# Kernel optimization log

Hardware: AMD Instinct MI355X
Metric: run time of the kernel (lower is better)

Reference implementation:

```python
import jax, jax.numpy as jnp
import numpy as np

N = 16384
D = 128
TOPK = 32


def setup_inputs() -> dict:
    key = jax.random.key(0)
    kx, kw = jax.random.split(key)
    x = jax.random.normal(kx, (N,), dtype=jnp.float32)  # unused by the module's forward
    W = jax.random.normal(kw, (N, D), dtype=jnp.float32)  # embedding table (learned param)
    return {"x": x, "W": W}


def reference(x, W):
    # adj = E @ E^T : [N, N] similarity matrix
    adj = W @ W.T
    # per-row top-K (torch.topk along dim=1)
    vals, idx = jax.lax.top_k(adj, TOPK)  # [N, K] each
    # dense_to_sparse emits nonzeros in row-major order -> sort columns within each row.
    order = jnp.argsort(idx, axis=1)
    idx_s = jnp.take_along_axis(idx, order, axis=1)
    vals_s = jnp.take_along_axis(vals, order, axis=1)
    rows = jnp.repeat(jnp.arange(N, dtype=idx_s.dtype), TOPK)
    edge_index = jnp.stack([rows, idx_s.reshape(-1)])  # [2, N*K]
    edge_values = vals_s.reshape(-1)  # [N*K]
    return edge_index, edge_values
```

## Files before the change

### kernel.cpp

```cpp
#include <hip/hip_runtime.h>
#include <hip/hip_bf16.h>
#include <hip/hip_fp16.h>


#define N_ROWS 16384
#define DIM    128
#define TOPK   32
#define NK     (N_ROWS * TOPK)
#define ZTAU   2.45f
#define DELTA  0.05f
#define CAPL   192
#define WCAP   48
#define RPB    32
#define NWAVE  8
#define CPS    256
#define NSTG   (N_ROWS / CPS)
#define W1BIN  0.15625f
#define W2BIN  0.00244140625f

using short8   = __attribute__((ext_vector_type(8)))  short;
using floatx16 = __attribute__((ext_vector_type(16))) float;

#define PK_ROWS 32
__global__ __launch_bounds__(256)
void pack_kernel(const float* __restrict__ W, unsigned short* __restrict__ FA,
                 unsigned short* __restrict__ FB, float* __restrict__ norm) {
    __shared__ float lds[PK_ROWS * 132];
    __shared__ float nrmS[PK_ROWS];
    const int t  = threadIdx.x;
    const int rb = blockIdx.x * PK_ROWS;

    const float4* src = (const float4*)(W + (size_t)rb * DIM);
    #pragma unroll
    for (int i = 0; i < 4; ++i) {
        const int f = t + 256 * i;
        const float4 v = src[f];
        const int r = f >> 5, j = f & 31;
        *(float4*)&lds[r * 132 + j * 4] = v;
        float ss = v.x * v.x + v.y * v.y + v.z * v.z + v.w * v.w;
        #pragma unroll
        for (int off = 1; off < 32; off <<= 1) ss += __shfl_xor(ss, off, 64);
        if (j == 0) nrmS[r] = sqrtf(ss);
    }
    __syncthreads();

    const size_t blkoff = (size_t)blockIdx.x * 8192;
    uint2* fa = (uint2*)((char*)FA + blkoff);
    uint2* fb = (uint2*)((char*)FB + blkoff);
    #pragma unroll
    for (int i = 0; i < 4; ++i) {
        const int p   = t + 256 * i;
        const int D   = 2 * p;
        const int q   = D >> 7, r31 = (D >> 2) & 31, w = D & 3;
        const float4 f4 = *(const float4*)&lds[r31 * 132 + q * 8 + w * 2];
        const float inv = 1.0f / nrmS[r31];
        __hip_bfloat16 b0 = __float2bfloat16(f4.x), b1 = __float2bfloat16(f4.y);
        __hip_bfloat16 b2 = __float2bfloat16(f4.z), b3 = __float2bfloat16(f4.w);
        fb[p] = make_uint2(
            (unsigned)(*(unsigned short*)&b0) | ((unsigned)(*(unsigned short*)&b1) << 16),
            (unsigned)(*(unsigned short*)&b2) | ((unsigned)(*(unsigned short*)&b3) << 16));
        __hip_bfloat16 a0 = __float2bfloat16(f4.x * inv), a1 = __float2bfloat16(f4.y * inv);
        __hip_bfloat16 a2 = __float2bfloat16(f4.z * inv), a3 = __float2bfloat16(f4.w * inv);
        fa[p] = make_uint2(
            (unsigned)(*(unsigned short*)&a0) | ((unsigned)(*(unsigned short*)&a1) << 16),
            (unsigned)(*(unsigned short*)&a2) | ((unsigned)(*(unsigned short*)&a3) << 16));
    }
    if (t < PK_ROWS) norm[rb + t] = nrmS[t];
}

__global__ __launch_bounds__(512, 4)
void fused_kernel(const unsigned short* __restrict__ FA,
                  const unsigned short* __restrict__ FB,
                  const float* __restrict__ W, const float* __restrict__ norm,
                  float* __restrict__ out) {
    __shared__ unsigned int scnt[RPB];
    __shared__ unsigned int candL[RPB * CAPL];
    __shared__ int          wcolS[NWAVE][WCAP];
    __shared__ double       dvalS[NWAVE][WCAP];
    __shared__ int          fcolS[NWAVE][TOPK];
    __shared__ float        fvalS[NWAVE][TOPK];
    __shared__ unsigned int wcntS[NWAVE], mcntS[NWAVE], fcntS[NWAVE];

    const int tid = threadIdx.x, lane = tid & 63, wid = tid >> 6;
    const int half = lane >> 5, l31 = lane & 31;
    const int rowbase = blockIdx.x * RPB;

    if (tid < RPB) scnt[tid] = 0u;
    __syncthreads();

    short8 afrag[8];
    {
        const char* ab = (const char*)FA + (size_t)(rowbase >> 5) * 8192
                       + half * 512 + l31 * 16;
        #pragma unroll
        for (int kt = 0; kt < 8; ++kt) afrag[kt] = *(const short8*)(ab + kt * 1024);
    }

    const int rbh = 4 * half;
    const char* bstream = (const char*)FB + (size_t)wid * 8192 + half * 512 + l31 * 16;
    const int s0 = (blockIdx.x * 37) & (NSTG - 1);

    for (int i = 0; i < NSTG; ++i) {
        const int s = (s0 + i) & (NSTG - 1);
        const char* bp = bstream + (size_t)s * 65536;
        short8 bA[4], bB[4];
        #pragma unroll
        for (int k = 0; k < 4; ++k) bA[k] = *(const short8*)(bp + k * 1024);
        #pragma unroll
        for (int k = 0; k < 4; ++k) bB[k] = *(const short8*)(bp + (4 + k) * 1024);
        floatx16 acc = (floatx16)0.0f;
        #pragma unroll
        for (int k = 0; k < 4; ++k)
            acc = __builtin_amdgcn_mfma_f32_32x32x16_bf16(afrag[k], bA[k], acc, 0, 0, 0);
        #pragma unroll
        for (int k = 0; k < 4; ++k)
            acc = __builtin_amdgcn_mfma_f32_32x32x16_bf16(afrag[4 + k], bB[k], acc, 0, 0, 0);

        const unsigned pcol = (unsigned)(s * CPS + wid * 32 + l31) << 16;
        #pragma unroll
        for (int r = 0; r < 16; ++r) {
            if (acc[r] > ZTAU) {
                const int rloc = rbh + (r & 3) + 8 * (r >> 2);
                unsigned slot = atomicAdd(&scnt[rloc], 1u);
                if (slot < CAPL)
                    candL[rloc * CAPL + slot] = pcol | __half_as_ushort(__float2half(acc[r]));
            }
        }
    }
    __syncthreads();

    unsigned int* histW = (unsigned int*)&dvalS[wid][0];
    for (int rr = 0; rr < 4; ++rr) {
        const int rloc = wid * 4 + rr;
        const int rowg = rowbase + rloc;
        int n = (int)scnt[rloc]; if (n > CAPL) n = CAPL;
        const unsigned int* cl = &candL[rloc * CAPL];

        if (lane == 0) { wcntS[wid] = 0u; mcntS[wid] = 0u; fcntS[wid] = 0u; }
        histW[lane] = 0u;
        for (int i = lane; i < n; i += 64) {
            const float v = __half2float(__ushort_as_half((unsigned short)(cl[i] & 0xFFFFu)));
            int b = (int)((v - ZTAU) * (1.0f / W1BIN));
            b = b < 0 ? 0 : (b > 63 ? 63 : b);
            atomicAdd(&histW[b], 1u);
        }
        unsigned sfx = histW[lane];
        #pragma unroll
        for (int off = 1; off < 64; off <<= 1) {
            unsigned u = __shfl_down(sfx, off, 64);
            if (lane + off < 64) sfx += u;
        }
        unsigned long long mk = __ballot(sfx >= (unsigned)TOPK);
        const int b1 = mk ? (63 - __clzll(mk)) : 0;
        unsigned Gup = __shfl(sfx, (b1 + 1) & 63, 64);
        if (b1 == 63) Gup = 0u;
        const float lo1 = ZTAU + (float)b1 * W1BIN;

        histW[lane] = 0u;
        for (int i = lane; i < n; i += 64) {
            const float v = __half2float(__ushort_as_half((unsigned short)(cl[i] & 0xFFFFu)));
            if (v >= lo1 && v < lo1 + W1BIN) {
                int b = (int)((v - lo1) * (1.0f / W2BIN));
                b = b < 0 ? 0 : (b > 63 ? 63 : b);
                atomicAdd(&histW[b], 1u);
            }
        }
        unsigned sfx2 = histW[lane];
        #pragma unroll
        for (int off = 1; off < 64; off <<= 1) {
            unsigned u = __shfl_down(sfx2, off, 64);
            if (lane + off < 64) sfx2 += u;
        }
        sfx2 += Gup;
        mk = __ballot(sfx2 >= (unsigned)TOPK);
        const int b2 = mk ? (63 - __clzll(mk)) : 0;
        const float vlo = lo1 + (float)b2 * W2BIN;
        const float vhi = vlo + W2BIN;

        for (int i = lane; i < n; i += 64) {
            const unsigned e = cl[i];
            const float v = __half2float(__ushort_as_half((unsigned short)(e & 0xFFFFu)));
            if (v > vhi + DELTA) {
                atomicAdd(&mcntS[wid], 1u);
            } else if (v >= vlo - DELTA) {
                unsigned u = atomicAdd(&wcntS[wid], 1u);
                if (u < WCAP) wcolS[wid][u] = (int)(e >> 16);
            }
        }
        const int m = (int)mcntS[wid];
        int wn = (int)wcntS[wid]; if (wn > WCAP) wn = WCAP;
        int need = TOPK - m; if (need < 0) need = 0;

        if (lane < wn) {
            const int col = wcolS[wid][lane] & (N_ROWS - 1);
            const float4* wa = (const float4*)(W + (size_t)rowg * DIM);
            const float4* wb = (const float4*)(W + (size_t)col * DIM);
            double d0 = 0, d1 = 0, d2 = 0, d3 = 0;
            #pragma unroll
            for (int k = 0; k < DIM / 4; ++k) {
                const float4 x = wa[k]; const float4 y = wb[k];
                d0 += (double)x.x * y.x; d1 += (double)x.y * y.y;
                d2 += (double)x.z * y.z; d3 += (double)x.w * y.w;
            }
            dvalS[wid][lane] = (d0 + d1) + (d2 + d3);
        }
        if (lane < wn) {
            const double dv = dvalS[wid][lane]; const int c = wcolS[wid][lane];
            int r = 0;
            for (int u = 0; u < wn; ++u) {
                const double du = dvalS[wid][u];
                r += (du > dv || (du == dv && wcolS[wid][u] < c)) ? 1 : 0;
            }
            if (r < need) {
                unsigned slot = atomicAdd(&fcntS[wid], 1u);
                if (slot < TOPK) { fcolS[wid][slot] = c; fvalS[wid][slot] = (float)dv; }
            }
        }
        const float nm = norm[rowg];
        for (int i = lane; i < n; i += 64) {
            const unsigned e = cl[i];
            const float v = __half2float(__ushort_as_half((unsigned short)(e & 0xFFFFu)));
            if (v > vhi + DELTA) {
                unsigned slot = atomicAdd(&fcntS[wid], 1u);
                if (slot < TOPK) { fcolS[wid][slot] = (int)(e >> 16); fvalS[wid][slot] = v * nm; }
            }
        }
        int fn = (int)fcntS[wid]; if (fn > TOPK) fn = TOPK;
        if (lane < fn) {
            const int c = fcolS[wid][lane];
            int pos = 0;
            for (int j = 0; j < fn; ++j) pos += (fcolS[wid][j] < c) ? 1 : 0;
            const size_t base = (size_t)rowg * TOPK + pos;
            out[base]                  = (float)rowg;
            out[NK + base]             = (float)c;
            out[2 * (size_t)NK + base] = fvalS[wid][lane];
        }
    }
}

extern "C" void kernel_launch(void* const* d_in, const int* in_sizes, int n_in,
                              void* d_out, int out_size, void* d_ws, size_t ws_size,
                              hipStream_t stream) {
    (void)in_sizes; (void)n_in; (void)out_size; (void)ws_size;
    const float* W   = (const float*)d_in[1];
    float*       out = (float*)d_out;

    char* ws = (char*)d_ws;
    unsigned short* FA   = (unsigned short*)ws;
    unsigned short* FB   = (unsigned short*)(ws + (size_t)4194304);
    float*          norm = (float*)(ws + (size_t)8388608);

    pack_kernel<<<N_ROWS / PK_ROWS, 256, 0, stream>>>(W, FA, FB, norm);
    fused_kernel<<<N_ROWS / RPB, 512, 0, stream>>>(FA, FB, W, norm, out);
}
```

Baseline: 208.5 us.

## Process 64 rows per block with two accumulators and double-buffered B loads

Each block now handles 64 query rows instead of 32, holding two sets of A fragments so every loaded B tile feeds two MFMA chains. This halves global B traffic per row. The next stage's B fragments are also prefetched into a second register buffer while the current stage computes. The cost is more registers and LDS per block (candidate lists double), which drops the occupancy target from 4 to 2 blocks per CU and halves the grid.

```diff
diff --git a/kernel.cpp b/kernel.cpp
--- a/kernel.cpp
+++ b/kernel.cpp
@@ -11,7 +11,7 @@
 #define DELTA  0.05f
 #define CAPL   192
 #define WCAP   48
-#define RPB    32
+#define RPB    64
 #define NWAVE  8
 #define CPS    256
 #define NSTG   (N_ROWS / CPS)
@@ -68,7 +68,7 @@
     if (t < PK_ROWS) norm[rb + t] = nrmS[t];
 }
 
-__global__ __launch_bounds__(512, 4)
+__global__ __launch_bounds__(512, 2)
 void fused_kernel(const unsigned short* __restrict__ FA,
                   const unsigned short* __restrict__ FB,
                   const float* __restrict__ W, const float* __restrict__ norm,
@@ -88,50 +88,73 @@
     if (tid < RPB) scnt[tid] = 0u;
     __syncthreads();
 
-    short8 afrag[8];
+    short8 afrag[16];
     {
         const char* ab = (const char*)FA + (size_t)(rowbase >> 5) * 8192
                        + half * 512 + l31 * 16;
         #pragma unroll
-        for (int kt = 0; kt < 8; ++kt) afrag[kt] = *(const short8*)(ab + kt * 1024);
+        for (int kt = 0; kt < 8; ++kt) afrag[kt]     = *(const short8*)(ab + kt * 1024);
+        #pragma unroll
+        for (int kt = 0; kt < 8; ++kt) afrag[8 + kt] = *(const short8*)(ab + 8192 + kt * 1024);
     }
 
     const int rbh = 4 * half;
     const char* bstream = (const char*)FB + (size_t)wid * 8192 + half * 512 + l31 * 16;
     const int s0 = (blockIdx.x * 37) & (NSTG - 1);
 
-    for (int i = 0; i < NSTG; ++i) {
-        const int s = (s0 + i) & (NSTG - 1);
-        const char* bp = bstream + (size_t)s * 65536;
-        short8 bA[4], bB[4];
-        #pragma unroll
-        for (int k = 0; k < 4; ++k) bA[k] = *(const short8*)(bp + k * 1024);
-        #pragma unroll
-        for (int k = 0; k < 4; ++k) bB[k] = *(const short8*)(bp + (4 + k) * 1024);
-        floatx16 acc = (floatx16)0.0f;
-        #pragma unroll
-        for (int k = 0; k < 4; ++k)
-            acc = __builtin_amdgcn_mfma_f32_32x32x16_bf16(afrag[k], bA[k], acc, 0, 0, 0);
-        #pragma unroll
-        for (int k = 0; k < 4; ++k)
-            acc = __builtin_amdgcn_mfma_f32_32x32x16_bf16(afrag[4 + k], bB[k], acc, 0, 0, 0);
-
-        const unsigned pcol = (unsigned)(s * CPS + wid * 32 + l31) << 16;
-        #pragma unroll
-        for (int r = 0; r < 16; ++r) {
-            if (acc[r] > ZTAU) {
-                const int rloc = rbh + (r & 3) + 8 * (r >> 2);
-                unsigned slot = atomicAdd(&scnt[rloc], 1u);
-                if (slot < CAPL)
-                    candL[rloc * CAPL + slot] = pcol | __half_as_ushort(__float2half(acc[r]));
-            }
-        }
-    }
+    short8 bu0[8], bu1[8];
+    {
+        const char* bp = bstream + (size_t)s0 * 65536;
+        #pragma unroll
+        for (int k = 0; k < 8; ++k) bu0[k] = *(const short8*)(bp + k * 1024);
+    }
+
+    #define STAGE(BC, BN, I)                                                   \
+    {                                                                          \
+        const int s  = (s0 + (I)) & (NSTG - 1);                                \
+        const int sn = (s0 + (I) + 1) & (NSTG - 1);                            \
+        const char* bpn = bstream + (size_t)sn * 65536;                        \
+        _Pragma("unroll")                                                      \
+        for (int k = 0; k < 8; ++k) BN[k] = *(const short8*)(bpn + k * 1024);  \
+        floatx16 accL = (floatx16)0.0f, accH = (floatx16)0.0f;                 \
+        _Pragma("unroll")                                                      \
+        for (int k = 0; k < 8; ++k) {                                          \
+            accL = __builtin_amdgcn_mfma_f32_32x32x16_bf16(afrag[k],     BC[k], accL, 0, 0, 0); \
+            accH = __builtin_amdgcn_mfma_f32_32x32x16_bf16(afrag[8 + k], BC[k], accH, 0, 0, 0); \
+        }                                                                      \
+        const unsigned pcol = (unsigned)(s * CPS + wid * 32 + l31) << 16;      \
+        _Pragma("unroll")                                                      \
+        for (int r = 0; r < 16; ++r) {                                         \
+            if (accL[r] > ZTAU) {                                              \
+                const int rloc = rbh + (r & 3) + 8 * (r >> 2);                 \
+                unsigned slot = atomicAdd(&scnt[rloc], 1u);                    \
+                if (slot < CAPL)                                               \
+                    candL[rloc * CAPL + slot] =                                \
+                        pcol | __half_as_ushort(__float2half(accL[r]));        \
+            }                                                                  \
+        }                                                                      \
+        _Pragma("unroll")                                                      \
+        for (int r = 0; r < 16; ++r) {                                         \
+            if (accH[r] > ZTAU) {                                              \
+                const int rloc = 32 + rbh + (r & 3) + 8 * (r >> 2);            \
+                unsigned slot = atomicAdd(&scnt[rloc], 1u);                    \
+                if (slot < CAPL)                                               \
+                    candL[rloc * CAPL + slot] =                                \
+                        pcol | __half_as_ushort(__float2half(accH[r]));        \
+            }                                                                  \
+        }                                                                      \
+    }
+
+    for (int i = 0; i < NSTG; i += 2) {
+        STAGE(bu0, bu1, i);
+        STAGE(bu1, bu0, i + 1);
+    }
+    #undef STAGE
     __syncthreads();
 
     unsigned int* histW = (unsigned int*)&dvalS[wid][0];
-    for (int rr = 0; rr < 4; ++rr) {
-        const int rloc = wid * 4 + rr;
+    for (int rr = 0; rr < 8; ++rr) {
+        const int rloc = wid * 8 + rr;
         const int rowg = rowbase + rloc;
         int n = (int)scnt[rloc]; if (n > CAPL) n = CAPL;
         const unsigned int* cl = &candL[rloc * CAPL];
```

Measured after the change: 236.2 us. 13.3% more time.

## Exploit Gram matrix symmetry with triangular tile pairs and global candidate lists

Applied to the files above, without the earlier changes.

Because W·Wᵀ is symmetric, only upper-triangular 256x256 tile pairs are computed, and each off-diagonal score is pushed as a candidate to both its row and its column through global atomics into per-row candidate buffers. A single unnormalized bf16 copy of W is used, with per-row thresholds scaled by the norm, replacing the separate normalized A copy. Selection moves into its own tail kernel that works from the global candidate lists. This roughly halves the MFMA work but adds global atomic traffic, an extra kernel launch, and candidate ordering that depends on scheduling.

```diff
diff --git a/kernel.cpp b/kernel.cpp
--- a/kernel.cpp
+++ b/kernel.cpp
@@ -11,10 +11,10 @@
 #define DELTA  0.05f
 #define CAPL   192
 #define WCAP   48
-#define RPB    32
 #define NWAVE  8
-#define CPS    256
-#define NSTG   (N_ROWS / CPS)
+#define TILE   256
+#define NT     (N_ROWS / TILE)
+#define NPAIR  (NT * (NT + 1) / 2)
 #define W1BIN  0.15625f
 #define W2BIN  0.00244140625f
 
@@ -23,12 +23,16 @@
 
 #define PK_ROWS 32
 __global__ __launch_bounds__(256)
-void pack_kernel(const float* __restrict__ W, unsigned short* __restrict__ FA,
-                 unsigned short* __restrict__ FB, float* __restrict__ norm) {
+void pack_kernel(const float* __restrict__ W, unsigned short* __restrict__ F,
+                 float* __restrict__ norm, float* __restrict__ tau,
+                 unsigned int* __restrict__ gcnt) {
     __shared__ float lds[PK_ROWS * 132];
     __shared__ float nrmS[PK_ROWS];
     const int t  = threadIdx.x;
     const int rb = blockIdx.x * PK_ROWS;
+
+    { const int gid = blockIdx.x * 256 + t;
+      if (gid < N_ROWS) gcnt[gid] = 0u; }
 
     const float4* src = (const float4*)(W + (size_t)rb * DIM);
     #pragma unroll
@@ -45,36 +49,101 @@
     __syncthreads();
 
     const size_t blkoff = (size_t)blockIdx.x * 8192;
-    uint2* fa = (uint2*)((char*)FA + blkoff);
-    uint2* fb = (uint2*)((char*)FB + blkoff);
+    uint2* fb = (uint2*)((char*)F + blkoff);
     #pragma unroll
     for (int i = 0; i < 4; ++i) {
         const int p   = t + 256 * i;
         const int D   = 2 * p;
         const int q   = D >> 7, r31 = (D >> 2) & 31, w = D & 3;
         const float4 f4 = *(const float4*)&lds[r31 * 132 + q * 8 + w * 2];
-        const float inv = 1.0f / nrmS[r31];
         __hip_bfloat16 b0 = __float2bfloat16(f4.x), b1 = __float2bfloat16(f4.y);
         __hip_bfloat16 b2 = __float2bfloat16(f4.z), b3 = __float2bfloat16(f4.w);
         fb[p] = make_uint2(
             (unsigned)(*(unsigned short*)&b0) | ((unsigned)(*(unsigned short*)&b1) << 16),
             (unsigned)(*(unsigned short*)&b2) | ((unsigned)(*(unsigned short*)&b3) << 16));
-        __hip_bfloat16 a0 = __float2bfloat16(f4.x * inv), a1 = __float2bfloat16(f4.y * inv);
-        __hip_bfloat16 a2 = __float2bfloat16(f4.z * inv), a3 = __float2bfloat16(f4.w * inv);
-        fa[p] = make_uint2(
-            (unsigned)(*(unsigned short*)&a0) | ((unsigned)(*(unsigned short*)&a1) << 16),
-            (unsigned)(*(unsigned short*)&a2) | ((unsigned)(*(unsigned short*)&a3) << 16));
-    }
-    if (t < PK_ROWS) norm[rb + t] = nrmS[t];
+    }
+    if (t < PK_ROWS) { norm[rb + t] = nrmS[t]; tau[rb + t] = ZTAU * nrmS[t]; }
 }
 
 __global__ __launch_bounds__(512, 4)
-void fused_kernel(const unsigned short* __restrict__ FA,
-                  const unsigned short* __restrict__ FB,
-                  const float* __restrict__ W, const float* __restrict__ norm,
-                  float* __restrict__ out) {
-    __shared__ unsigned int scnt[RPB];
-    __shared__ unsigned int candL[RPB * CAPL];
+void score_kernel(const unsigned short* __restrict__ F,
+                  const float* __restrict__ tau,
+                  unsigned int* __restrict__ gcnt,
+                  unsigned int* __restrict__ gcand) {
+    __shared__ unsigned short Bs[TILE * DIM];
+
+    const int tid = threadIdx.x, lane = tid & 63, wid = tid >> 6;
+    const int half = lane >> 5, l31 = lane & 31;
+
+    int ti = 0, rem = blockIdx.x;
+    while (rem >= NT - ti) { rem -= NT - ti; ++ti; }
+    const int tj = ti + rem;
+    const int Rbase = ti * TILE, Cbase = tj * TILE;
+    const bool offdiag = (ti != tj);
+
+    {
+        const short8* src = (const short8*)((const char*)F + (size_t)(Cbase >> 5) * 8192);
+        short8* dst = (short8*)Bs;
+        #pragma unroll
+        for (int c = 0; c < 8; ++c) dst[tid + 512 * c] = src[tid + 512 * c];
+    }
+
+    short8 afrag[8];
+    {
+        const char* ab = (const char*)F + (size_t)((Rbase >> 5) + wid) * 8192
+                       + half * 512 + l31 * 16;
+        #pragma unroll
+        for (int k = 0; k < 8; ++k) afrag[k] = *(const short8*)(ab + k * 1024);
+    }
+
+    float rt[16];
+    #pragma unroll
+    for (int r = 0; r < 16; ++r)
+        rt[r] = tau[Rbase + wid * 32 + 4 * half + (r & 3) + 8 * (r >> 2)];
+
+    __syncthreads();
+
+    #pragma unroll 1
+    for (int cb = 0; cb < 8; ++cb) {
+        const int col = Cbase + cb * 32 + l31;
+        const float ctv = offdiag ? tau[col] : 3.0e38f;
+
+        short8 bf[8];
+        const char* bb = (const char*)Bs + cb * 8192 + half * 512 + l31 * 16;
+        #pragma unroll
+        for (int k = 0; k < 8; ++k) bf[k] = *(const short8*)(bb + k * 1024);
+
+        floatx16 acc = (floatx16)0.0f;
+        #pragma unroll
+        for (int k = 0; k < 8; ++k)
+            acc = __builtin_amdgcn_mfma_f32_32x32x16_bf16(afrag[k], bf[k], acc, 0, 0, 0);
+
+        #pragma unroll
+        for (int r = 0; r < 16; ++r) {
+            const float raw = acc[r];
+            if (raw > fminf(rt[r], ctv)) {
+                const int row = Rbase + wid * 32 + 4 * half + (r & 3) + 8 * (r >> 2);
+                const unsigned short h = __half_as_ushort(__float2half(raw));
+                if (raw > rt[r]) {
+                    unsigned slot = atomicAdd(&gcnt[row], 1u);
+                    if (slot < CAPL)
+                        gcand[(size_t)row * CAPL + slot] = ((unsigned)col << 16) | h;
+                }
+                if (raw > ctv) {
+                    unsigned slot = atomicAdd(&gcnt[col], 1u);
+                    if (slot < CAPL)
+                        gcand[(size_t)col * CAPL + slot] = ((unsigned)row << 16) | h;
+                }
+            }
+        }
+    }
+}
+
+__global__ __launch_bounds__(512)
+void tail_kernel(const unsigned int* __restrict__ gcnt,
+                 const unsigned int* __restrict__ gcand,
+                 const float* __restrict__ W, const float* __restrict__ norm,
+                 float* __restrict__ out) {
     __shared__ int          wcolS[NWAVE][WCAP];
     __shared__ double       dvalS[NWAVE][WCAP];
     __shared__ int          fcolS[NWAVE][TOPK];
@@ -82,159 +151,111 @@
     __shared__ unsigned int wcntS[NWAVE], mcntS[NWAVE], fcntS[NWAVE];
 
     const int tid = threadIdx.x, lane = tid & 63, wid = tid >> 6;
-    const int half = lane >> 5, l31 = lane & 31;
-    const int rowbase = blockIdx.x * RPB;
-
-    if (tid < RPB) scnt[tid] = 0u;
-    __syncthreads();
-
-    short8 afrag[8];
-    {
-        const char* ab = (const char*)FA + (size_t)(rowbase >> 5) * 8192
-                       + half * 512 + l31 * 16;
-        #pragma unroll
-        for (int kt = 0; kt < 8; ++kt) afrag[kt] = *(const short8*)(ab + kt * 1024);
-    }
-
-    const int rbh = 4 * half;
-    const char* bstream = (const char*)FB + (size_t)wid * 8192 + half * 512 + l31 * 16;
-    const int s0 = (blockIdx.x * 37) & (NSTG - 1);
-
-    for (int i = 0; i < NSTG; ++i) {
-        const int s = (s0 + i) & (NSTG - 1);
-        const char* bp = bstream + (size_t)s * 65536;
-        short8 bA[4], bB[4];
-        #pragma unroll
-        for (int k = 0; k < 4; ++k) bA[k] = *(const short8*)(bp + k * 1024);
-        #pragma unroll
-        for (int k = 0; k < 4; ++k) bB[k] = *(const short8*)(bp + (4 + k) * 1024);
-        floatx16 acc = (floatx16)0.0f;
-        #pragma unroll
-        for (int k = 0; k < 4; ++k)
-            acc = __builtin_amdgcn_mfma_f32_32x32x16_bf16(afrag[k], bA[k], acc, 0, 0, 0);
-        #pragma unroll
-        for (int k = 0; k < 4; ++k)
-            acc = __builtin_amdgcn_mfma_f32_32x32x16_bf16(afrag[4 + k], bB[k], acc, 0, 0, 0);
-
-        const unsigned pcol = (unsigned)(s * CPS + wid * 32 + l31) << 16;
-        #pragma unroll
-        for (int r = 0; r < 16; ++r) {
-            if (acc[r] > ZTAU) {
-                const int rloc = rbh + (r & 3) + 8 * (r >> 2);
-                unsigned slot = atomicAdd(&scnt[rloc], 1u);
-                if (slot < CAPL)
-                    candL[rloc * CAPL + slot] = pcol | __half_as_ushort(__float2half(acc[r]));
-            }
-        }
-    }
-    __syncthreads();
+    const int rowg = blockIdx.x * NWAVE + wid;
+    const float inv = 1.0f / norm[rowg];
+
+    int n = (int)gcnt[rowg]; if (n > CAPL) n = CAPL;
+    const unsigned int* cl = &gcand[(size_t)rowg * CAPL];
 
     unsigned int* histW = (unsigned int*)&dvalS[wid][0];
-    for (int rr = 0; rr < 4; ++rr) {
-        const int rloc = wid * 4 + rr;
-        const int rowg = rowbase + rloc;
-        int n = (int)scnt[rloc]; if (n > CAPL) n = CAPL;
-        const unsigned int* cl = &candL[rloc * CAPL];
-
-        if (lane == 0) { wcntS[wid] = 0u; mcntS[wid] = 0u; fcntS[wid] = 0u; }
-        histW[lane] = 0u;
-        for (int i = lane; i < n; i += 64) {
-            const float v = __half2float(__ushort_as_half((unsigned short)(cl[i] & 0xFFFFu)));
-            int b = (int)((v - ZTAU) * (1.0f / W1BIN));
+
+    if (lane == 0) { wcntS[wid] = 0u; mcntS[wid] = 0u; fcntS[wid] = 0u; }
+    histW[lane] = 0u;
+    for (int i = lane; i < n; i += 64) {
+        const float v = __half2float(__ushort_as_half((unsigned short)(cl[i] & 0xFFFFu))) * inv;
+        int b = (int)((v - ZTAU) * (1.0f / W1BIN));
+        b = b < 0 ? 0 : (b > 63 ? 63 : b);
+        atomicAdd(&histW[b], 1u);
+    }
+    unsigned sfx = histW[lane];
+    #pragma unroll
+    for (int off = 1; off < 64; off <<= 1) {
+        unsigned u = __shfl_down(sfx, off, 64);
+        if (lane + off < 64) sfx += u;
+    }
+    unsigned long long mk = __ballot(sfx >= (unsigned)TOPK);
+    const int b1 = mk ? (63 - __clzll(mk)) : 0;
+    unsigned Gup = __shfl(sfx, (b1 + 1) & 63, 64);
+    if (b1 == 63) Gup = 0u;
+    const float lo1 = ZTAU + (float)b1 * W1BIN;
+
+    histW[lane] = 0u;
+    for (int i = lane; i < n; i += 64) {
+        const float v = __half2float(__ushort_as_half((unsigned short)(cl[i] & 0xFFFFu))) * inv;
+        if (v >= lo1 && v < lo1 + W1BIN) {
+            int b = (int)((v - lo1) * (1.0f / W2BIN));
             b = b < 0 ? 0 : (b > 63 ? 63 : b);
             atomicAdd(&histW[b], 1u);
         }
-        unsigned sfx = histW[lane];
-        #pragma unroll
-        for (int off = 1; off < 64; off <<= 1) {
-            unsigned u = __shfl_down(sfx, off, 64);
-            if (lane + off < 64) sfx += u;
-        }
-        unsigned long long mk = __ballot(sfx >= (unsigned)TOPK);
-        const int b1 = mk ? (63 - __clzll(mk)) : 0;
-        unsigned Gup = __shfl(sfx, (b1 + 1) & 63, 64);
-        if (b1 == 63) Gup = 0u;
-        const float lo1 = ZTAU + (float)b1 * W1BIN;
-
-        histW[lane] = 0u;
-        for (int i = lane; i < n; i += 64) {
-            const float v = __half2float(__ushort_as_half((unsigned short)(cl[i] & 0xFFFFu)));
-            if (v >= lo1 && v < lo1 + W1BIN) {
-                int b = (int)((v - lo1) * (1.0f / W2BIN));
-                b = b < 0 ? 0 : (b > 63 ? 63 : b);
-                atomicAdd(&histW[b], 1u);
-            }
-        }
-        unsigned sfx2 = histW[lane];
-        #pragma unroll
-        for (int off = 1; off < 64; off <<= 1) {
-            unsigned u = __shfl_down(sfx2, off, 64);
-            if (lane + off < 64) sfx2 += u;
-        }
-        sfx2 += Gup;
-        mk = __ballot(sfx2 >= (unsigned)TOPK);
-        const int b2 = mk ? (63 - __clzll(mk)) : 0;
-        const float vlo = lo1 + (float)b2 * W2BIN;
-        const float vhi = vlo + W2BIN;
-
-        for (int i = lane; i < n; i += 64) {
-            const unsigned e = cl[i];
-            const float v = __half2float(__ushort_as_half((unsigned short)(e & 0xFFFFu)));
-            if (v > vhi + DELTA) {
-                atomicAdd(&mcntS[wid], 1u);
-            } else if (v >= vlo - DELTA) {
-                unsigned u = atomicAdd(&wcntS[wid], 1u);
-                if (u < WCAP) wcolS[wid][u] = (int)(e >> 16);
-            }
-        }
-        const int m = (int)mcntS[wid];
-        int wn = (int)wcntS[wid]; if (wn > WCAP) wn = WCAP;
-        int need = TOPK - m; if (need < 0) need = 0;
-
-        if (lane < wn) {
-            const int col = wcolS[wid][lane] & (N_ROWS - 1);
-            const float4* wa = (const float4*)(W + (size_t)rowg * DIM);
-            const float4* wb = (const float4*)(W + (size_t)col * DIM);
-            double d0 = 0, d1 = 0, d2 = 0, d3 = 0;
-            #pragma unroll
-            for (int k = 0; k < DIM / 4; ++k) {
-                const float4 x = wa[k]; const float4 y = wb[k];
-                d0 += (double)x.x * y.x; d1 += (double)x.y * y.y;
-                d2 += (double)x.z * y.z; d3 += (double)x.w * y.w;
-            }
-            dvalS[wid][lane] = (d0 + d1) + (d2 + d3);
-        }
-        if (lane < wn) {
-            const double dv = dvalS[wid][lane]; const int c = wcolS[wid][lane];
-            int r = 0;
-            for (int u = 0; u < wn; ++u) {
-                const double du = dvalS[wid][u];
-                r += (du > dv || (du == dv && wcolS[wid][u] < c)) ? 1 : 0;
-            }
-            if (r < need) {
-                unsigned slot = atomicAdd(&fcntS[wid], 1u);
-                if (slot < TOPK) { fcolS[wid][slot] = c; fvalS[wid][slot] = (float)dv; }
-            }
-        }
-        const float nm = norm[rowg];
-        for (int i = lane; i < n; i += 64) {
-            const unsigned e = cl[i];
-            const float v = __half2float(__ushort_as_half((unsigned short)(e & 0xFFFFu)));
-            if (v > vhi + DELTA) {
-                unsigned slot = atomicAdd(&fcntS[wid], 1u);
-                if (slot < TOPK) { fcolS[wid][slot] = (int)(e >> 16); fvalS[wid][slot] = v * nm; }
-            }
-        }
-        int fn = (int)fcntS[wid]; if (fn > TOPK) fn = TOPK;
-        if (lane < fn) {
-            const int c = fcolS[wid][lane];
-            int pos = 0;
-            for (int j = 0; j < fn; ++j) pos += (fcolS[wid][j] < c) ? 1 : 0;
-            const size_t base = (size_t)rowg * TOPK + pos;
-            out[base]                  = (float)rowg;
-            out[NK + base]             = (float)c;
-            out[2 * (size_t)NK + base] = fvalS[wid][lane];
-        }
+    }
+    unsigned sfx2 = histW[lane];
+    #pragma unroll
+    for (int off = 1; off < 64; off <<= 1) {
+        unsigned u = __shfl_down(sfx2, off, 64);
+        if (lane + off < 64) sfx2 += u;
+    }
+    sfx2 += Gup;
+    mk = __ballot(sfx2 >= (unsigned)TOPK);
+    const int b2 = mk ? (63 - __clzll(mk)) : 0;
+    const float vlo = lo1 + (float)b2 * W2BIN;
+    const float vhi = vlo + W2BIN;
+
+    for (int i = lane; i < n; i += 64) {
+        const unsigned e = cl[i];
+        const float v = __half2float(__ushort_as_half((unsigned short)(e & 0xFFFFu))) * inv;
+        if (v > vhi + DELTA) {
+            atomicAdd(&mcntS[wid], 1u);
+        } else if (v >= vlo - DELTA) {
+            unsigned u = atomicAdd(&wcntS[wid], 1u);
+            if (u < WCAP) wcolS[wid][u] = (int)(e >> 16);
+        }
+    }
+    const int m = (int)mcntS[wid];
+    int wn = (int)wcntS[wid]; if (wn > WCAP) wn = WCAP;
+    int need = TOPK - m; if (need < 0) need = 0;
+
+    if (lane < wn) {
+        const int col = wcolS[wid][lane] & (N_ROWS - 1);
+        const float4* wa = (const float4*)(W + (size_t)rowg * DIM);
+        const float4* wb = (const float4*)(W + (size_t)col * DIM);
+        double d0 = 0, d1 = 0, d2 = 0, d3 = 0;
+        #pragma unroll
+        for (int k = 0; k < DIM / 4; ++k) {
+            const float4 x = wa[k]; const float4 y = wb[k];
+            d0 += (double)x.x * y.x; d1 += (double)x.y * y.y;
+            d2 += (double)x.z * y.z; d3 += (double)x.w * y.w;
+        }
+        dvalS[wid][lane] = (d0 + d1) + (d2 + d3);
+    }
+    if (lane < wn) {
+        const double dv = dvalS[wid][lane]; const int c = wcolS[wid][lane];
+        int r = 0;
+        for (int u = 0; u < wn; ++u) {
+            const double du = dvalS[wid][u];
+            r += (du > dv || (du == dv && wcolS[wid][u] < c)) ? 1 : 0;
+        }
+        if (r < need) {
+            unsigned slot = atomicAdd(&fcntS[wid], 1u);
+            if (slot < TOPK) { fcolS[wid][slot] = c; fvalS[wid][slot] = (float)dv; }
+        }
+    }
+    for (int i = lane; i < n; i += 64) {
+        const unsigned e = cl[i];
+        const float vr = __half2float(__ushort_as_half((unsigned short)(e & 0xFFFFu)));
+        if (vr * inv > vhi + DELTA) {
+            unsigned slot = atomicAdd(&fcntS[wid], 1u);
+            if (slot < TOPK) { fcolS[wid][slot] = (int)(e >> 16); fvalS[wid][slot] = vr; }
+        }
+    }
+    int fn = (int)fcntS[wid]; if (fn > TOPK) fn = TOPK;
+    if (lane < fn) {
+        const int c = fcolS[wid][lane];
+        int pos = 0;
+        for (int j = 0; j < fn; ++j) pos += (fcolS[wid][j] < c) ? 1 : 0;
+        const size_t base = (size_t)rowg * TOPK + pos;
+        out[base]                  = (float)rowg;
+        out[NK + base]             = (float)c;
+        out[2 * (size_t)NK + base] = fvalS[wid][lane];
     }
 }
 
@@ -246,10 +267,13 @@
     float*       out = (float*)d_out;
 
     char* ws = (char*)d_ws;
-    unsigned short* FA   = (unsigned short*)ws;
-    unsigned short* FB   = (unsigned short*)(ws + (size_t)4194304);
-    float*          norm = (float*)(ws + (size_t)8388608);
-
-    pack_kernel<<<N_ROWS / PK_ROWS, 256, 0, stream>>>(W, FA, FB, norm);
-    fused_kernel<<<N_ROWS / RPB, 512, 0, stream>>>(FA, FB, W, norm, out);
-}
+    unsigned short* F    = (unsigned short*)ws;
+    float*          norm = (float*)(ws + (size_t)4194304);
+    float*          tau  = (float*)(ws + (size_t)4194304 + 65536);
+    unsigned int*   gcnt = (unsigned int*)(ws + (size_t)4194304 + 131072);
+    unsigned int*   gcand= (unsigned int*)(ws + (size_t)4194304 + 196608);
+
+    pack_kernel<<<N_ROWS / PK_ROWS, 256, 0, stream>>>(W, F, norm, tau, gcnt);
+    score_kernel<<<NPAIR, 512, 0, stream>>>(F, tau, gcnt, gcand);
+    tail_kernel<<<N_ROWS / NWAVE, 512, 0, stream>>>(gcnt, gcand, W, norm, out);
+}
```

After: 372.7 us. +78.7%, slower.
